# Kernel optimization log

Measured on AMD Instinct MI355X. Metric: run time of the kernel, lower is better.

Reference implementation:

```python
import jax, jax.numpy as jnp
import numpy as np

B, T, I, H = 2048, 512, 9, 56


def _lstm_layer(x, w_ih, w_hh, b_ih, b_hh):
    """Single LSTM layer, batch_first x: [B, T, in] -> [B, T, H].
    PyTorch gate order: i, f, g, o."""
    # Precompute input projections for all timesteps in one GEMM: [B, T, 4H]
    xp = jnp.einsum('bti,gi->btg', x, w_ih) + b_ih + b_hh
    xp_t = jnp.transpose(xp, (1, 0, 2))  # [T, B, 4H]
    h0 = jnp.zeros((x.shape[0], w_hh.shape[1]), dtype=x.dtype)
    c0 = jnp.zeros_like(h0)

    def step(carry, xt):
        h, c = carry
        gates = xt + h @ w_hh.T  # [B, 4H]
        i, f, g, o = jnp.split(gates, 4, axis=-1)
        i = jax.nn.sigmoid(i)
        f = jax.nn.sigmoid(f)
        g = jnp.tanh(g)
        o = jax.nn.sigmoid(o)
        c = f * c + i * g
        h = o * jnp.tanh(c)
        return (h, c), h

    _, hs = jax.lax.scan(step, (h0, c0), xp_t)  # hs: [T, B, H]
    return jnp.transpose(hs, (1, 0, 2))  # [B, T, H]


def setup_inputs() -> dict:
    key = jax.random.key(0)
    ks = jax.random.split(key, 13)
    s_in = 1.0 / np.sqrt(H)
    inp = {
        'x': jax.random.normal(ks[0], (B, T, I), dtype=jnp.float32),
        'w_ih0': jax.random.uniform(ks[1], (4 * H, I), jnp.float32, -s_in, s_in),
        'w_hh0': jax.random.uniform(ks[2], (4 * H, H), jnp.float32, -s_in, s_in),
        'b_ih0': jax.random.uniform(ks[3], (4 * H,), jnp.float32, -s_in, s_in),
        'b_hh0': jax.random.uniform(ks[4], (4 * H,), jnp.float32, -s_in, s_in),
        'w_ih1': jax.random.uniform(ks[5], (4 * H, H), jnp.float32, -s_in, s_in),
        'w_hh1': jax.random.uniform(ks[6], (4 * H, H), jnp.float32, -s_in, s_in),
        'b_ih1': jax.random.uniform(ks[7], (4 * H,), jnp.float32, -s_in, s_in),
        'b_hh1': jax.random.uniform(ks[8], (4 * H,), jnp.float32, -s_in, s_in),
        'fc1_w': jax.random.uniform(ks[9], (H // 2, H), jnp.float32, -s_in, s_in),
        'fc1_b': jax.random.uniform(ks[10], (H // 2,), jnp.float32, -s_in, s_in),
        'fc2_w': jax.random.uniform(ks[11], (1, H // 2), jnp.float32, -0.2, 0.2),
        'fc2_b': jax.random.uniform(ks[12], (1,), jnp.float32, -0.2, 0.2),
    }
    return inp


def reference(x, w_ih0, w_hh0, b_ih0, b_hh0, w_ih1, w_hh1, b_ih1, b_hh1,
              fc1_w, fc1_b, fc2_w, fc2_b):
    h = _lstm_layer(x, w_ih0, w_hh0, b_ih0, b_hh0)   # [B, T, H]
    h = _lstm_layer(h, w_ih1, w_hh1, b_ih1, b_hh1)   # [B, T, H]
    last = h[:, -1]                                   # [B, H]
    y = jax.nn.relu(last @ fc1_w.T + fc1_b)           # [B, H//2]
    return y @ fc2_w.T + fc2_b                        # [B, 1]
```

## Files before the change

### kernel.cpp

```cpp
#include <hip/hip_runtime.h>
#include <stdint.h>

#define T_LEN 512
#define IN0   9
#define H     56
#define BG    8
#define NW    14
#define NTH   (NW * 64)
#define NBLK  256
#define SROW  20

typedef __attribute__((ext_vector_type(8))) short bfrag;
typedef __attribute__((ext_vector_type(4))) float ffrag;

#define MFMA(a,b,c) __builtin_amdgcn_mfma_f32_16x16x32_bf16((a),(b),(c),0,0,0)

__device__ __forceinline__ uint32_t bf16hi(float x) {
  uint32_t u = __float_as_uint(x);
  return (u + 0x7FFFu + ((u >> 16) & 1u)) & 0xFFFF0000u;
}
__device__ __forceinline__ void split_bf16(float x, short& hs, short& ls) {
  uint32_t hb = bf16hi(x);
  float lf = x - __uint_as_float(hb);
  hs = (short)(hb >> 16);
  ls = (short)(bf16hi(lf) >> 16);
}
__device__ __forceinline__ float rcp_f(float v)  { return __builtin_amdgcn_rcpf(v); }
__device__ __forceinline__ float sigm_f(float v) { return rcp_f(1.0f + __expf(-v)); }
__device__ __forceinline__ float tanh_f(float v) { return 1.0f - 2.0f * rcp_f(1.0f + __expf(2.0f * v)); }

__global__ __launch_bounds__(NTH, 4)
void lstm_mfma4(const float* __restrict__ x,
                const float* __restrict__ w_ih0, const float* __restrict__ w_hh0,
                const float* __restrict__ b_ih0, const float* __restrict__ b_hh0,
                const float* __restrict__ w_ih1, const float* __restrict__ w_hh1,
                const float* __restrict__ b_ih1, const float* __restrict__ b_hh1,
                const float* __restrict__ fc1_w, const float* __restrict__ fc1_b,
                const float* __restrict__ fc2_w, const float* __restrict__ fc2_b,
                float* __restrict__ out)
{
  __shared__ __align__(16) short sA[4][1024];
  __shared__ __align__(16) float sS[2][NW][16][SROW];
  __shared__ float sF[BG * H];
  __shared__ float sY[BG * 28];

  const int tid  = threadIdx.x;
  const int lane = tid & 63;
  const int w    = tid >> 6;
  const int c16  = lane & 15;
  const int quad = lane >> 4;

  const int np   = 16 * w + c16;
  const int jb   = np >> 2, gb = np & 3;
  const int wrow = gb * H + jb;

  for (int i = tid; i < (int)(sizeof(sA) / 4); i += NTH) ((int*)sA)[i] = 0;

  bfrag B0h[2], B0l[2], Buh[2], Bul[2], Bhh[2], Bhl[2];
  #pragma unroll
  for (int s = 0; s < 2; ++s) {
    union { short sh[8]; bfrag v; } a0h, a0l, auh, aul, ahh, ahl;
    #pragma unroll
    for (int jj = 0; jj < 8; ++jj) {
      const int k = 32 * s + quad * 8 + jj;
      const float w0 = (k < H) ? w_hh0[wrow * H + k] : w_ih0[wrow * IN0 + (k - 56)];
      const float wu = (k < H) ? w_ih1[wrow * H + k] : 0.0f;
      const float wh = (k < H) ? w_hh1[wrow * H + k] : 0.0f;
      split_bf16(w0, a0h.sh[jj], a0l.sh[jj]);
      split_bf16(wu, auh.sh[jj], aul.sh[jj]);
      split_bf16(wh, ahh.sh[jj], ahl.sh[jj]);
    }
    B0h[s] = a0h.v; B0l[s] = a0l.v;
    Buh[s] = auh.v; Bul[s] = aul.v;
    Bhh[s] = ahh.v; Bhl[s] = ahl.v;
  }

  const float b0v = (quad < 2) ? (b_ih0[wrow] + b_hh0[wrow]) : 0.0f;
  const float b1v = (quad < 2) ? (b_ih1[wrow] + b_hh1[wrow]) : 0.0f;
  const ffrag bias0f = { b0v, b0v, b0v, b0v };
  const ffrag bias1f = { b1v, b1v, b1v, b1v };
  const ffrag zerof  = { 0.f, 0.f, 0.f, 0.f };

  const int half = lane >> 5;
  const int bq   = (lane >> 2) & 7;
  const int jlc  = lane & 3;
  const int aj   = 4 * w + jlc;

  float wx8a[4];
  #pragma unroll
  for (int g = 0; g < 4; ++g)
    wx8a[g] = half ? w_ih0[(g * H + aj) * IN0 + 8] : 0.0f;

  const int kk   = aj & 31;
  const int offE = (aj >> 5) * 512 + ((kk >> 3) * 16 + bq) * 8 + (kk & 7);
  short* const hst0 = &sA[0][0] + (half ? 0 : 3 * 1024) + offE;
  short* const hst1 = &sA[0][0] + (half ? 1 * 1024 : 2 * 1024) + offE;
  const int offX = 512 + (48 + bq) * 8 + 2 * jlc;
  short* const xst0 = &sA[0][0] + offX;
  short* const xst1 = &sA[1][0] + offX;
  float* const scW = &sS[0][w][0][0] + quad * 4 * SROW + c16;
  float* const sdW = &sS[1][w][0][0] + quad * 4 * SROW + c16;
  const float* const srd = &sS[half][w][0][0] + bq * SROW + 4 * jlc;
  const short* const sAr = &sA[0][0];

  const size_t xbase = (size_t)(blockIdx.x * BG + bq) * T_LEN * IN0;
  const float* xp8 = x + xbase + 8;
  const float* xps = x + xbase + IN0 + 2 * jlc;

  float cst = 0.f;
  __syncthreads();

  if (w == 0) {
    const float xa = xps[-IN0], xb = xps[1 - IN0];
    if (half) {
      short ah, al2, bh, bl2;
      split_bf16(xa, ah, al2); split_bf16(xb, bh, bl2);
      *(uint32_t*)xst0        = (uint16_t)ah  | ((uint32_t)(uint16_t)bh  << 16);
      *(uint32_t*)(xst0 + 64) = (uint16_t)al2 | ((uint32_t)(uint16_t)bl2 << 16);
    }
  }
  __syncthreads();

  {
    bfrag A0 = *(const bfrag*)(sAr + lane * 8);
    bfrag A1 = *(const bfrag*)(sAr + 512 + lane * 8);
    ffrag aA = MFMA(A0, B0h[0], bias0f);
    aA = MFMA(A1, B0h[1], aA);
    aA = MFMA(A0, B0l[0], aA);
    aA = MFMA(A1, B0l[1], aA);
    sdW[0] = aA[0]; sdW[SROW] = aA[1]; sdW[2 * SROW] = aA[2]; sdW[3 * SROW] = aA[3];
    const float x8v = xp8[0];
    xp8 += IN0;
    if (half) {
      const float4 ghi = *(const float4*)srd;
      const float4 glo = *(const float4*)(srd + 8 * SROW);
      const float gi = fmaf(wx8a[0], x8v, ghi.x + glo.x);
      const float gf = fmaf(wx8a[1], x8v, ghi.y + glo.y);
      const float gg = fmaf(wx8a[2], x8v, ghi.z + glo.z);
      const float go = fmaf(wx8a[3], x8v, ghi.w + glo.w);
      const float iv = sigm_f(gi), fv = sigm_f(gf), gv = tanh_f(gg), ov = sigm_f(go);
      cst = fmaf(fv, cst, iv * gv);
      const float hv = ov * tanh_f(cst);
      short hs, hl; split_bf16(hv, hs, hl);
      hst1[0] = hs; hst1[64] = hl;
    }
    if (w == 0) {
      const float xa = xps[0], xb = xps[1];
      if (half) {
        short ah, al2, bh, bl2;
        split_bf16(xa, ah, al2); split_bf16(xb, bh, bl2);
        *(uint32_t*)xst1        = (uint16_t)ah  | ((uint32_t)(uint16_t)bh  << 16);
        *(uint32_t*)(xst1 + 64) = (uint16_t)al2 | ((uint32_t)(uint16_t)bl2 << 16);
      }
    }
    xps += IN0;
    __syncthreads();
  }

#define REGION(RR, L0PART, XSTG, LASTR)                                         \
  {                                                                             \
    bfrag U0 = *(const bfrag*)(sAr + (RR ^ 1) * 1024 + lane * 8);               \
    bfrag U1 = *(const bfrag*)(sAr + (RR ^ 1) * 1024 + 512 + lane * 8);         \
    bfrag H0 = *(const bfrag*)(sAr + (2 + RR) * 1024 + lane * 8);               \
    bfrag H1 = *(const bfrag*)(sAr + (2 + RR) * 1024 + 512 + lane * 8);         \
    float x8v = 0.0f;                                                           \
    if (L0PART) { x8v = xp8[0]; xp8 += IN0; }                                   \
    ffrag aU = MFMA(U0, Buh[0], bias1f);                                        \
    aU = MFMA(U1, Buh[1], aU);                                                  \
    aU = MFMA(U0, Bul[0], aU);                                                  \
    aU = MFMA(U1, Bul[1], aU);                                                  \
    ffrag aH = MFMA(H0, Bhh[0], zerof);                                         \
    aH = MFMA(H1, Bhh[1], aH);                                                  \
    aH = MFMA(H0, Bhl[0], aH);                                                  \
    aH = MFMA(H1, Bhl[1], aH);                                                  \
    scW[0]        = aU[0] + aH[0];                                              \
    scW[SROW]     = aU[1] + aH[1];                                              \
    scW[2 * SROW] = aU[2] + aH[2];                                              \
    scW[3 * SROW] = aU[3] + aH[3];                                              \
    if (L0PART) {                                                               \
      ffrag aA = MFMA(U0, B0h[0], bias0f);                                      \
      aA = MFMA(U1, B0h[1], aA);                                                \
      aA = MFMA(U0, B0l[0], aA);                                                \
      aA = MFMA(U1, B0l[1], aA);                                                \
      sdW[0] = aA[0]; sdW[SROW] = aA[1];                                        \
      sdW[2 * SROW] = aA[2]; sdW[3 * SROW] = aA[3];                             \
    }                                                                           \
    if (!LASTR) {                                                               \
      const float4 ghi = *(const float4*)srd;                                   \
      const float4 glo = *(const float4*)(srd + 8 * SROW);                      \
      const float gi = fmaf(wx8a[0], x8v, ghi.x + glo.x);                       \
      const float gf = fmaf(wx8a[1], x8v, ghi.y + glo.y);                       \
      const float gg = fmaf(wx8a[2], x8v, ghi.z + glo.z);                       \
      const float go = fmaf(wx8a[3], x8v, ghi.w + glo.w);                       \
      const float iv = sigm_f(gi), fv = sigm_f(gf);                             \
      const float gv = tanh_f(gg), ov = sigm_f(go);                             \
      cst = fmaf(fv, cst, iv * gv);                                             \
      const float hv = ov * tanh_f(cst);                                        \
      short hs, hl; split_bf16(hv, hs, hl);                                     \
      short* hb = (RR == 0) ? hst0 : hst1;                                      \
      hb[0] = hs; hb[64] = hl;                                                  \
    } else if (half == 0) {                                                     \
      const float4 ghi = *(const float4*)srd;                                   \
      const float4 glo = *(const float4*)(srd + 8 * SROW);                      \
      const float gi = ghi.x + glo.x;                                           \
      const float gf = ghi.y + glo.y;                                           \
      const float gg = ghi.z + glo.z;                                           \
      const float go = ghi.w + glo.w;                                           \
      const float iv = sigm_f(gi), fv = sigm_f(gf);                             \
      const float gv = tanh_f(gg), ov = sigm_f(go);                             \
      cst = fmaf(fv, cst, iv * gv);                                             \
      sF[bq * H + aj] = ov * tanh_f(cst);                                       \
    }                                                                           \
    if (XSTG) {                                                                 \
      if (w == 0) {                                                             \
        const float xa = xps[0], xb = xps[1];                                   \
        if (half) {                                                             \
          short ah, al2, bh, bl2;                                               \
          split_bf16(xa, ah, al2); split_bf16(xb, bh, bl2);                     \
          short* xb_ = (RR == 0) ? xst0 : xst1;                                 \
          *(uint32_t*)xb_        = (uint16_t)ah  | ((uint32_t)(uint16_t)bh  << 16); \
          *(uint32_t*)(xb_ + 64) = (uint16_t)al2 | ((uint32_t)(uint16_t)bl2 << 16); \
        }                                                                       \
      }                                                                         \
      xps += IN0;                                                               \
    }                                                                           \
    __syncthreads();                                                            \
  }

  for (int it = 0; it < 255; ++it) {
    REGION(0, 1, 1, 0)
    REGION(1, 1, 1, 0)
  }
  REGION(0, 1, 0, 0)
  REGION(1, 0, 0, 1)
#undef REGION

  if (tid < 28 * BG) {
    const int m  = tid >> 3;
    const int bb = tid & 7;
    float acc = fc1_b[m];
    const float4* w4 = (const float4*)(fc1_w + m * H);
    const float4* h4 = (const float4*)(sF + bb * H);
    #pragma unroll
    for (int qq = 0; qq < H / 4; ++qq) {
      const float4 wv4 = w4[qq], hv4 = h4[qq];
      acc = fmaf(wv4.x, hv4.x, acc);
      acc = fmaf(wv4.y, hv4.y, acc);
      acc = fmaf(wv4.z, hv4.z, acc);
      acc = fmaf(wv4.w, hv4.w, acc);
    }
    sY[bb * 28 + m] = fmaxf(acc, 0.0f);
  }
  __syncthreads();
  if (tid < BG) {
    float acc = fc2_b[0];
    #pragma unroll
    for (int m = 0; m < 28; ++m)
      acc = fmaf(fc2_w[m], sY[tid * 28 + m], acc);
    out[blockIdx.x * BG + tid] = acc;
  }
}

extern "C" void kernel_launch(void* const* d_in, const int* in_sizes, int n_in,
                              void* d_out, int out_size, void* d_ws, size_t ws_size,
                              hipStream_t stream)
{
  const float* x     = (const float*)d_in[0];
  const float* w_ih0 = (const float*)d_in[1];
  const float* w_hh0 = (const float*)d_in[2];
  const float* b_ih0 = (const float*)d_in[3];
  const float* b_hh0 = (const float*)d_in[4];
  const float* w_ih1 = (const float*)d_in[5];
  const float* w_hh1 = (const float*)d_in[6];
  const float* b_ih1 = (const float*)d_in[7];
  const float* b_hh1 = (const float*)d_in[8];
  const float* fc1_w = (const float*)d_in[9];
  const float* fc1_b = (const float*)d_in[10];
  const float* fc2_w = (const float*)d_in[11];
  const float* fc2_b = (const float*)d_in[12];
  float* out = (float*)d_out;

  lstm_mfma4<<<NBLK, NTH, 0, stream>>>(
      x, w_ih0, w_hh0, b_ih0, b_hh0, w_ih1, w_hh1, b_ih1, b_hh1,
      fc1_w, fc1_b, fc2_w, fc2_b, out);
}
```

Before: 474.1 us.

## Swap MFMA operand roles so gate outputs stay in registers, drop LDS staging

Transposes the MFMA so the weight fragments become the A operand and hidden states the B operand. Each lane then holds all four gates for one hidden unit and batch row, and the two K-halves are combined with a lane shuffle rather than written to and read back from a shared-memory scratch buffer. Layer-1 input and recurrent contributions are also chained into a single accumulator, removing an add. This cuts LDS traffic and shared-memory footprint per timestep, but every lane now runs the activation math for either layer, and the code adds per-step shuffles and selects.

```diff
diff --git a/kernel.cpp b/kernel.cpp
--- a/kernel.cpp
+++ b/kernel.cpp
@@ -8,7 +8,6 @@
 #define NW    14
 #define NTH   (NW * 64)
 #define NBLK  256
-#define SROW  20
 
 typedef __attribute__((ext_vector_type(8))) short bfrag;
 typedef __attribute__((ext_vector_type(4))) float ffrag;
@@ -30,7 +29,7 @@
 __device__ __forceinline__ float tanh_f(float v) { return 1.0f - 2.0f * rcp_f(1.0f + __expf(2.0f * v)); }
 
 __global__ __launch_bounds__(NTH, 4)
-void lstm_mfma4(const float* __restrict__ x,
+void lstm_mfma5(const float* __restrict__ x,
                 const float* __restrict__ w_ih0, const float* __restrict__ w_hh0,
                 const float* __restrict__ b_ih0, const float* __restrict__ b_hh0,
                 const float* __restrict__ w_ih1, const float* __restrict__ w_hh1,
@@ -39,8 +38,7 @@
                 const float* __restrict__ fc2_w, const float* __restrict__ fc2_b,
                 float* __restrict__ out)
 {
-  __shared__ __align__(16) short sA[4][1024];
-  __shared__ __align__(16) float sS[2][NW][16][SROW];
+  __shared__ __align__(16) short sB[4][1024];
   __shared__ float sF[BG * H];
   __shared__ float sY[BG * 28];
 
@@ -54,7 +52,7 @@
   const int jb   = np >> 2, gb = np & 3;
   const int wrow = gb * H + jb;
 
-  for (int i = tid; i < (int)(sizeof(sA) / 4); i += NTH) ((int*)sA)[i] = 0;
+  for (int i = tid; i < (int)(sizeof(sB) / 4); i += NTH) ((int*)sB)[i] = 0;
 
   bfrag B0h[2], B0l[2], Buh[2], Bul[2], Bhh[2], Bhl[2];
   #pragma unroll
@@ -75,154 +73,150 @@
     Bhh[s] = ahh.v; Bhl[s] = ahl.v;
   }
 
-  const float b0v = (quad < 2) ? (b_ih0[wrow] + b_hh0[wrow]) : 0.0f;
-  const float b1v = (quad < 2) ? (b_ih1[wrow] + b_hh1[wrow]) : 0.0f;
-  const ffrag bias0f = { b0v, b0v, b0v, b0v };
-  const ffrag bias1f = { b1v, b1v, b1v, b1v };
-  const ffrag zerof  = { 0.f, 0.f, 0.f, 0.f };
-
-  const int half = lane >> 5;
-  const int bq   = (lane >> 2) & 7;
-  const int jlc  = lane & 3;
-  const int aj   = 4 * w + jlc;
-
+  const int j4 = 4 * w + quad;
+  ffrag bias0f, bias1f;
+  #pragma unroll
+  for (int r = 0; r < 4; ++r) {
+    const float v0 = b_ih0[r * H + j4] + b_hh0[r * H + j4];
+    const float v1 = b_ih1[r * H + j4] + b_hh1[r * H + j4];
+    bias0f[r] = (c16 < 8) ? v0 : 0.0f;
+    bias1f[r] = (c16 < 8) ? v1 : 0.0f;
+  }
+
+  const int lay = (lane >> 3) & 1;
+  const int b   = lane & 7;
   float wx8a[4];
   #pragma unroll
-  for (int g = 0; g < 4; ++g)
-    wx8a[g] = half ? w_ih0[(g * H + aj) * IN0 + 8] : 0.0f;
-
-  const int kk   = aj & 31;
-  const int offE = (aj >> 5) * 512 + ((kk >> 3) * 16 + bq) * 8 + (kk & 7);
-  short* const hst0 = &sA[0][0] + (half ? 0 : 3 * 1024) + offE;
-  short* const hst1 = &sA[0][0] + (half ? 1 * 1024 : 2 * 1024) + offE;
-  const int offX = 512 + (48 + bq) * 8 + 2 * jlc;
-  short* const xst0 = &sA[0][0] + offX;
-  short* const xst1 = &sA[1][0] + offX;
-  float* const scW = &sS[0][w][0][0] + quad * 4 * SROW + c16;
-  float* const sdW = &sS[1][w][0][0] + quad * 4 * SROW + c16;
-  const float* const srd = &sS[half][w][0][0] + bq * SROW + 4 * jlc;
-  const short* const sAr = &sA[0][0];
-
-  const size_t xbase = (size_t)(blockIdx.x * BG + bq) * T_LEN * IN0;
-  const float* xp8 = x + xbase + 8;
-  const float* xps = x + xbase + IN0 + 2 * jlc;
+  for (int r = 0; r < 4; ++r)
+    wx8a[r] = lay ? w_ih0[(r * H + j4) * IN0 + 8] : 0.0f;
+
+  const int kk   = j4 & 31;
+  const int offE = (j4 >> 5) * 512 + ((kk >> 3) * 16 + b) * 8 + (kk & 7);
+  short* const hp0 = &sB[0][0] + (lay ? 0 : 3 * 1024) + offE;
+  short* const hp1 = &sB[0][0] + (lay ? 1 * 1024 : 2 * 1024) + offE;
+
+  const int shalf = lane >> 5;
+  const int sbq   = (lane >> 2) & 7;
+  const int sjlc  = lane & 3;
+  const int offX  = 512 + (48 + sbq) * 8 + 2 * sjlc;
+  short* const xst0 = &sB[0][0] + offX;
+  short* const xst1 = &sB[1][0] + offX;
+  const short* const sBr = &sB[0][0];
+
+  const float* xp8 = x + (size_t)(blockIdx.x * BG + b)   * T_LEN * IN0 + 8;
+  const float* xps = x + (size_t)(blockIdx.x * BG + sbq) * T_LEN * IN0 + IN0 + 2 * sjlc;
 
   float cst = 0.f;
   __syncthreads();
 
-  if (w == 0) {
+  if (w == 0 && shalf) {
     const float xa = xps[-IN0], xb = xps[1 - IN0];
-    if (half) {
-      short ah, al2, bh, bl2;
-      split_bf16(xa, ah, al2); split_bf16(xb, bh, bl2);
-      *(uint32_t*)xst0        = (uint16_t)ah  | ((uint32_t)(uint16_t)bh  << 16);
-      *(uint32_t*)(xst0 + 64) = (uint16_t)al2 | ((uint32_t)(uint16_t)bl2 << 16);
-    }
+    short ah, al2, bh, bl2;
+    split_bf16(xa, ah, al2); split_bf16(xb, bh, bl2);
+    *(uint32_t*)xst0        = (uint16_t)ah  | ((uint32_t)(uint16_t)bh  << 16);
+    *(uint32_t*)(xst0 + 64) = (uint16_t)al2 | ((uint32_t)(uint16_t)bl2 << 16);
   }
   __syncthreads();
 
   {
-    bfrag A0 = *(const bfrag*)(sAr + lane * 8);
-    bfrag A1 = *(const bfrag*)(sAr + 512 + lane * 8);
-    ffrag aA = MFMA(A0, B0h[0], bias0f);
-    aA = MFMA(A1, B0h[1], aA);
-    aA = MFMA(A0, B0l[0], aA);
-    aA = MFMA(A1, B0l[1], aA);
-    sdW[0] = aA[0]; sdW[SROW] = aA[1]; sdW[2 * SROW] = aA[2]; sdW[3 * SROW] = aA[3];
+    bfrag U0 = *(const bfrag*)(sBr + lane * 8);
+    bfrag U1 = *(const bfrag*)(sBr + 512 + lane * 8);
+    ffrag a0 = MFMA(B0h[0], U0, bias0f);
+    a0 = MFMA(B0h[1], U1, a0);
+    a0 = MFMA(B0l[0], U0, a0);
+    a0 = MFMA(B0l[1], U1, a0);
     const float x8v = xp8[0];
     xp8 += IN0;
-    if (half) {
-      const float4 ghi = *(const float4*)srd;
-      const float4 glo = *(const float4*)(srd + 8 * SROW);
-      const float gi = fmaf(wx8a[0], x8v, ghi.x + glo.x);
-      const float gf = fmaf(wx8a[1], x8v, ghi.y + glo.y);
-      const float gg = fmaf(wx8a[2], x8v, ghi.z + glo.z);
-      const float go = fmaf(wx8a[3], x8v, ghi.w + glo.w);
+    float s0[4];
+    #pragma unroll
+    for (int r = 0; r < 4; ++r) s0[r] = a0[r] + __shfl_xor(a0[r], 8);
+    if (lay) {
+      const float gi = fmaf(wx8a[0], x8v, s0[0]);
+      const float gf = fmaf(wx8a[1], x8v, s0[1]);
+      const float gg = fmaf(wx8a[2], x8v, s0[2]);
+      const float go = fmaf(wx8a[3], x8v, s0[3]);
       const float iv = sigm_f(gi), fv = sigm_f(gf), gv = tanh_f(gg), ov = sigm_f(go);
       cst = fmaf(fv, cst, iv * gv);
       const float hv = ov * tanh_f(cst);
       short hs, hl; split_bf16(hv, hs, hl);
-      hst1[0] = hs; hst1[64] = hl;
-    }
-    if (w == 0) {
+      hp1[0] = hs; hp1[64] = hl;
+    }
+    if (w == 0 && shalf) {
       const float xa = xps[0], xb = xps[1];
-      if (half) {
-        short ah, al2, bh, bl2;
-        split_bf16(xa, ah, al2); split_bf16(xb, bh, bl2);
-        *(uint32_t*)xst1        = (uint16_t)ah  | ((uint32_t)(uint16_t)bh  << 16);
-        *(uint32_t*)(xst1 + 64) = (uint16_t)al2 | ((uint32_t)(uint16_t)bl2 << 16);
-      }
-    }
-    xps += IN0;
+      short ah, al2, bh, bl2;
+      split_bf16(xa, ah, al2); split_bf16(xb, bh, bl2);
+      *(uint32_t*)xst1        = (uint16_t)ah  | ((uint32_t)(uint16_t)bh  << 16);
+      *(uint32_t*)(xst1 + 64) = (uint16_t)al2 | ((uint32_t)(uint16_t)bl2 << 16);
+      xps += IN0;
+    }
     __syncthreads();
   }
 
 #define REGION(RR, L0PART, XSTG, LASTR)                                         \
   {                                                                             \
-    bfrag U0 = *(const bfrag*)(sAr + (RR ^ 1) * 1024 + lane * 8);               \
-    bfrag U1 = *(const bfrag*)(sAr + (RR ^ 1) * 1024 + 512 + lane * 8);         \
-    bfrag H0 = *(const bfrag*)(sAr + (2 + RR) * 1024 + lane * 8);               \
-    bfrag H1 = *(const bfrag*)(sAr + (2 + RR) * 1024 + 512 + lane * 8);         \
+    bfrag U0 = *(const bfrag*)(sBr + (RR ^ 1) * 1024 + lane * 8);               \
+    bfrag U1 = *(const bfrag*)(sBr + (RR ^ 1) * 1024 + 512 + lane * 8);         \
+    bfrag H0 = *(const bfrag*)(sBr + (2 + RR) * 1024 + lane * 8);               \
+    bfrag H1 = *(const bfrag*)(sBr + (2 + RR) * 1024 + 512 + lane * 8);         \
     float x8v = 0.0f;                                                           \
     if (L0PART) { x8v = xp8[0]; xp8 += IN0; }                                   \
-    ffrag aU = MFMA(U0, Buh[0], bias1f);                                        \
-    aU = MFMA(U1, Buh[1], aU);                                                  \
-    aU = MFMA(U0, Bul[0], aU);                                                  \
-    aU = MFMA(U1, Bul[1], aU);                                                  \
-    ffrag aH = MFMA(H0, Bhh[0], zerof);                                         \
-    aH = MFMA(H1, Bhh[1], aH);                                                  \
-    aH = MFMA(H0, Bhl[0], aH);                                                  \
-    aH = MFMA(H1, Bhl[1], aH);                                                  \
-    scW[0]        = aU[0] + aH[0];                                              \
-    scW[SROW]     = aU[1] + aH[1];                                              \
-    scW[2 * SROW] = aU[2] + aH[2];                                              \
-    scW[3 * SROW] = aU[3] + aH[3];                                              \
+    ffrag a1 = MFMA(Bhh[0], H0, bias1f);                                        \
+    a1 = MFMA(Bhh[1], H1, a1);                                                  \
+    a1 = MFMA(Bhl[0], H0, a1);                                                  \
+    a1 = MFMA(Bhl[1], H1, a1);                                                  \
+    a1 = MFMA(Buh[0], U0, a1);                                                  \
+    a1 = MFMA(Buh[1], U1, a1);                                                  \
+    a1 = MFMA(Bul[0], U0, a1);                                                  \
+    a1 = MFMA(Bul[1], U1, a1);                                                  \
+    ffrag a0 = a1;                                                              \
     if (L0PART) {                                                               \
-      ffrag aA = MFMA(U0, B0h[0], bias0f);                                      \
-      aA = MFMA(U1, B0h[1], aA);                                                \
-      aA = MFMA(U0, B0l[0], aA);                                                \
-      aA = MFMA(U1, B0l[1], aA);                                                \
-      sdW[0] = aA[0]; sdW[SROW] = aA[1];                                        \
-      sdW[2 * SROW] = aA[2]; sdW[3 * SROW] = aA[3];                             \
+      a0 = MFMA(B0h[0], U0, bias0f);                                            \
+      a0 = MFMA(B0h[1], U1, a0);                                                \
+      a0 = MFMA(B0l[0], U0, a0);                                                \
+      a0 = MFMA(B0l[1], U1, a0);                                                \
     }                                                                           \
     if (!LASTR) {                                                               \
-      const float4 ghi = *(const float4*)srd;                                   \
-      const float4 glo = *(const float4*)(srd + 8 * SROW);                      \
-      const float gi = fmaf(wx8a[0], x8v, ghi.x + glo.x);                       \
-      const float gf = fmaf(wx8a[1], x8v, ghi.y + glo.y);                       \
-      const float gg = fmaf(wx8a[2], x8v, ghi.z + glo.z);                       \
-      const float go = fmaf(wx8a[3], x8v, ghi.w + glo.w);                       \
+      float s1[4], s0[4];                                                       \
+      _Pragma("unroll")                                                         \
+      for (int r = 0; r < 4; ++r) s1[r] = a1[r] + __shfl_xor(a1[r], 8);         \
+      _Pragma("unroll")                                                         \
+      for (int r = 0; r < 4; ++r) s0[r] = a0[r] + __shfl_xor(a0[r], 8);         \
+      const float g0s = lay ? s0[0] : s1[0];                                    \
+      const float g1s = lay ? s0[1] : s1[1];                                    \
+      const float g2s = lay ? s0[2] : s1[2];                                    \
+      const float g3s = lay ? s0[3] : s1[3];                                    \
+      const float gi = fmaf(wx8a[0], x8v, g0s);                                 \
+      const float gf = fmaf(wx8a[1], x8v, g1s);                                 \
+      const float gg = fmaf(wx8a[2], x8v, g2s);                                 \
+      const float go = fmaf(wx8a[3], x8v, g3s);                                 \
       const float iv = sigm_f(gi), fv = sigm_f(gf);                             \
       const float gv = tanh_f(gg), ov = sigm_f(go);                             \
       cst = fmaf(fv, cst, iv * gv);                                             \
       const float hv = ov * tanh_f(cst);                                        \
       short hs, hl; split_bf16(hv, hs, hl);                                     \
-      short* hb = (RR == 0) ? hst0 : hst1;                                      \
+      short* hb = (RR == 0) ? hp0 : hp1;                                        \
       hb[0] = hs; hb[64] = hl;                                                  \
-    } else if (half == 0) {                                                     \
-      const float4 ghi = *(const float4*)srd;                                   \
-      const float4 glo = *(const float4*)(srd + 8 * SROW);                      \
-      const float gi = ghi.x + glo.x;                                           \
-      const float gf = ghi.y + glo.y;                                           \
-      const float gg = ghi.z + glo.z;                                           \
-      const float go = ghi.w + glo.w;                                           \
-      const float iv = sigm_f(gi), fv = sigm_f(gf);                             \
-      const float gv = tanh_f(gg), ov = sigm_f(go);                             \
-      cst = fmaf(fv, cst, iv * gv);                                             \
-      sF[bq * H + aj] = ov * tanh_f(cst);                                       \
+    } else {                                                                    \
+      float s1[4];                                                              \
+      _Pragma("unroll")                                                         \
+      for (int r = 0; r < 4; ++r) s1[r] = a1[r] + __shfl_xor(a1[r], 8);         \
+      if (lay == 0) {                                                           \
+        const float iv = sigm_f(s1[0]), fv = sigm_f(s1[1]);                     \
+        const float gv = tanh_f(s1[2]), ov = sigm_f(s1[3]);                     \
+        cst = fmaf(fv, cst, iv * gv);                                           \
+        sF[b * H + j4] = ov * tanh_f(cst);                                      \
+      }                                                                         \
     }                                                                           \
     if (XSTG) {                                                                 \
-      if (w == 0) {                                                             \
+      if (w == 0 && shalf) {                                                    \
         const float xa = xps[0], xb = xps[1];                                   \
-        if (half) {                                                             \
-          short ah, al2, bh, bl2;                                               \
-          split_bf16(xa, ah, al2); split_bf16(xb, bh, bl2);                     \
-          short* xb_ = (RR == 0) ? xst0 : xst1;                                 \
-          *(uint32_t*)xb_        = (uint16_t)ah  | ((uint32_t)(uint16_t)bh  << 16); \
-          *(uint32_t*)(xb_ + 64) = (uint16_t)al2 | ((uint32_t)(uint16_t)bl2 << 16); \
-        }                                                                       \
+        short ah, al2, bh, bl2;                                                 \
+        split_bf16(xa, ah, al2); split_bf16(xb, bh, bl2);                       \
+        short* xb_ = (RR == 0) ? xst0 : xst1;                                   \
+        *(uint32_t*)xb_        = (uint16_t)ah  | ((uint32_t)(uint16_t)bh  << 16); \
+        *(uint32_t*)(xb_ + 64) = (uint16_t)al2 | ((uint32_t)(uint16_t)bl2 << 16); \
+        xps += IN0;                                                             \
       }                                                                         \
-      xps += IN0;                                                               \
     }                                                                           \
     __syncthreads();                                                            \
   }
@@ -280,7 +274,7 @@
   const float* fc2_b = (const float*)d_in[12];
   float* out = (float*)d_out;
 
-  lstm_mfma4<<<NBLK, NTH, 0, stream>>>(
+  lstm_mfma5<<<NBLK, NTH, 0, stream>>>(
       x, w_ih0, w_hh0, b_ih0, b_hh0, w_ih1, w_hh1, b_ih1, b_hh1,
       fc1_w, fc1_b, fc2_w, fc2_b, out);
 }
```

New measurement: 480.4 us. Within noise of the previous version (+1.3%).
